# Kernel tuning notes

Hardware: AMD Instinct MI355X
Metric: run time of the kernel (lower is better)

The kernel has to match this reference:

```python
import jax, jax.numpy as jnp
import numpy as np

B, N, H, S, C = 32, 64, 128, 100, 16
SIGMA = 0.5  # perturbations.perturbed default noise scale


def setup_inputs() -> dict:
    key = jax.random.key(0)
    ks = jax.random.split(key, 8)
    x = jax.random.normal(ks[0], (B, N, H), jnp.float32)
    a = (jax.random.uniform(ks[1], (B, N, N)) < 0.1).astype(jnp.float32)
    adj = jnp.maximum(a, jnp.swapaxes(a, -1, -2))  # symmetric binary adjacency
    counts = jax.random.randint(ks[2], (B,), N // 2, N + 1)
    mask = jnp.arange(N)[None, :] < counts[:, None]
    sc = 1.0 / np.sqrt(H).astype(np.float32)
    W1 = jax.random.normal(ks[3], (H, H), jnp.float32) * sc
    b1 = jnp.zeros((H,), jnp.float32)
    W2 = jax.random.normal(ks[4], (H, H), jnp.float32) * sc
    b2 = jnp.zeros((H,), jnp.float32)
    cW1 = jax.random.normal(ks[5], (H, H), jnp.float32) * sc
    cb1 = jnp.zeros((H,), jnp.float32)
    cW2 = jax.random.normal(ks[6], (H, C), jnp.float32) * sc
    cb2 = jnp.zeros((C,), jnp.float32)
    noise = jax.random.normal(ks[7], (S * B, N, H), jnp.float32)
    return dict(x=x, adj=adj, mask=mask, W1=W1, b1=b1, W2=W2, b2=b2,
                cW1=cW1, cb1=cb1, cW2=cW2, cb2=cb2, noise=noise, num_samples=S)


def _gcn(x, adj, mask, W, b):
    # DenseGCNConv: set diag to 1, symmetric-normalize, propagate, mask.
    h = x @ W
    n = adj.shape[-1]
    eye = jnp.eye(n, dtype=bool)
    a = jnp.where(eye, 1.0, adj)
    d = jnp.clip(a.sum(-1), 1.0, None) ** -0.5
    a = d[..., :, None] * a * d[..., None, :]
    out = a @ h + b
    return out * mask[..., None].astype(out.dtype)


def _perturbed_clustering(x_all, adj_all, mask_all, cW1, cb1, cW2, cb2):
    BS, n, h = x_all.shape
    # concept MLP + argmax
    logits = jax.nn.relu(x_all @ cW1 + cb1) @ cW2 + cb2
    concepts = jnp.argmax(logits, axis=-1)  # [BS, n]
    same = concepts[:, :, None] == concepts[:, None, :]
    adj_c = jnp.where(same, adj_all, 0.0)
    # connected components via min-label propagation (scipy-order relabel)
    edge = (adj_c > 0) & mask_all[:, :, None] & mask_all[:, None, :]
    labels0 = jnp.where(mask_all, jnp.arange(n, dtype=jnp.int32), n)

    def body(_, labels):
        neigh = jnp.min(jnp.where(edge, labels[:, None, :], n), axis=-1)
        return jnp.minimum(labels, neigh)

    roots = jax.lax.fori_loop(0, n, body, labels0)  # min node idx of component
    present = jnp.zeros((BS, n + 1), jnp.int32).at[
        jnp.arange(BS)[:, None], roots].max(mask_all.astype(jnp.int32))
    rank = jnp.cumsum(present[:, :n], axis=-1)  # 1-based compact id per root
    assignments = jnp.where(
        mask_all,
        jnp.take_along_axis(rank, jnp.minimum(roots, n - 1), axis=-1), 0)
    # scatter-reduce pooling; segment ids flatten (batch, cluster); slot 0 = masked
    seg = (jnp.arange(BS, dtype=jnp.int32)[:, None] * (n + 1) + assignments).reshape(-1)
    x_new = jax.ops.segment_sum(x_all.reshape(BS * n, h), seg,
                                num_segments=BS * (n + 1)).reshape(BS, n + 1, h)[:, 1:]
    row = jax.ops.segment_max(adj_all.reshape(BS * n, n), seg,
                              num_segments=BS * (n + 1)).reshape(BS, n + 1, n)[:, 1:]
    row = jnp.maximum(row, 0.0)  # torch_scatter max includes zero-init
    colsrc = jnp.swapaxes(row, 1, 2).reshape(BS * n, n)
    adj_new = jax.ops.segment_max(colsrc, seg,
                                  num_segments=BS * (n + 1)).reshape(BS, n + 1, n)[:, 1:]
    adj_new = jnp.maximum(jnp.swapaxes(adj_new, 1, 2), 0.0)
    num_clusters = jnp.max(assignments, axis=-1)
    mask_new = jnp.arange(n)[None, :] < num_clusters[:, None]
    return x_new, adj_new, mask_new, assignments


def reference(x, adj, mask, W1, b1, W2, b2, cW1, cb1, cW2, cb2, noise, num_samples):
    # embedding GCN stack
    xe = jax.nn.relu(_gcn(x, adj, mask, W1, b1))
    x_emb = jax.nn.relu(_gcn(xe, adj, mask, W2, b2))
    Bb, n, h = x_emb.shape
    # perturbed replication (sample-major layout, matching final reshape(S, -1, ...))
    adj_all = jnp.tile(adj, (num_samples, 1, 1))
    mask_all = jnp.tile(mask, (num_samples, 1))
    x_all = jnp.tile(x_emb, (num_samples, 1, 1)) + SIGMA * noise
    x_new, adj_new, mask_new, assignments = _perturbed_clustering(
        x_all, adj_all, mask_all, cW1, cb1, cW2, cb2)
    # perturbed expectation for x_new; explicit mean/max in forward for adj/mask
    x_new = x_new.reshape(num_samples, Bb, n, h).mean(axis=0)
    adj_new = adj_new.reshape(num_samples, Bb, n, n).mean(axis=0)
    mask_new = jnp.max(mask_new.reshape(num_samples, Bb, n), axis=0)
    return x_new, adj_new, assignments, x_emb, mask_new
```

## Files before the change

### kernel.cpp

```cpp
#include <hip/hip_runtime.h>
#include <cstdint>

#define B_ 32
#define N_ 64
#define H_ 128
#define S_ 100
#define C_ 16
#define SIGMA_ 0.5f

#define OFF_XNEW 0
#define OFF_ADJN 262144
#define OFF_ASGN 393216
#define OFF_XEMB 598016
#define OFF_MSKN 860160

__device__ __forceinline__ int read_mask_elem(const void* mp, int idx) {
    const unsigned int* u = (const unsigned int*)mp;
    const unsigned int w0 = u[0], w1 = u[1];
    if (w0 == 1u) {
        if (w1 == 1u) return ((const int*)mp)[idx] != 0;
        return ((const int*)mp)[2 * idx] != 0;
    }
    if (w0 == 0x3f800000u) return ((const float*)mp)[idx] != 0.0f;
    if (w0 == 0u) return ((const double*)mp)[idx] != 0.0;
    return ((const unsigned char*)mp)[idx] != 0;
}

__global__ __launch_bounds__(256) void gcn_kernel(
    const float* __restrict__ x, const float* __restrict__ adj,
    const void* __restrict__ maskp,
    const float* __restrict__ W1, const float* __restrict__ b1,
    const float* __restrict__ W2, const float* __restrict__ b2,
    float* __restrict__ out,
    unsigned long long* __restrict__ abits_ws,
    unsigned long long* __restrict__ mbits_ws)
{
    const int b = blockIdx.x;
    const int t = threadIdx.x;
    __shared__ float Xs[N_][130];
    __shared__ float Hs[N_][130];
    __shared__ float An[N_][65];
    __shared__ float dsh[N_];
    __shared__ unsigned long long mb_sh;

    if (t < 64) {
        const int mv = read_mask_elem(maskp, b * N_ + t);
        const unsigned long long bal = __ballot(mv != 0);
        if (t == 0) { mb_sh = bal; mbits_ws[b] = bal; }
    }
    for (int row = (t >> 6); row < N_; row += 4) {
        const int j = t & 63;
        const float v = adj[((size_t)b * N_ + row) * N_ + j];
        const unsigned long long bal = __ballot(v > 0.0f);
        if (j == 0) abits_ws[b * N_ + row] = bal;
        An[row][j] = (row == j) ? 1.0f : v;
    }
    __syncthreads();
    if (t < 64) {
        float s = 0.0f;
        for (int j = 0; j < N_; ++j) s += An[t][j];
        if (s < 1.0f) s = 1.0f;
        dsh[t] = 1.0f / sqrtf(s);
    }
    __syncthreads();
    for (int e = t; e < N_ * N_; e += 256) {
        const int i = e >> 6, j = e & 63;
        An[i][j] *= dsh[i] * dsh[j];
    }
    for (int e = t; e < N_ * H_; e += 256)
        Xs[e >> 7][e & 127] = x[(size_t)b * N_ * H_ + e];
    __syncthreads();

    const int ng = t & 15, kg = t >> 4;
    const unsigned long long mb = mb_sh;

    {
        float acc[4][8] = {};
        for (int d = 0; d < H_; ++d) {
            float xv[4];
#pragma unroll
            for (int r = 0; r < 4; ++r) xv[r] = Xs[4 * ng + r][d];
            const float4 wa = *(const float4*)(W1 + d * H_ + 8 * kg);
            const float4 wb = *(const float4*)(W1 + d * H_ + 8 * kg + 4);
            const float wf[8] = {wa.x, wa.y, wa.z, wa.w, wb.x, wb.y, wb.z, wb.w};
#pragma unroll
            for (int j = 0; j < 8; ++j)
#pragma unroll
                for (int r = 0; r < 4; ++r) acc[r][j] += xv[r] * wf[j];
        }
#pragma unroll
        for (int r = 0; r < 4; ++r)
#pragma unroll
            for (int j = 0; j < 8; ++j) Hs[4 * ng + r][8 * kg + j] = acc[r][j];
    }
    __syncthreads();
    {
        float acc[4][8] = {};
        for (int j2 = 0; j2 < N_; ++j2) {
            float av[4];
#pragma unroll
            for (int r = 0; r < 4; ++r) av[r] = An[4 * ng + r][j2];
            float hv[8];
#pragma unroll
            for (int j = 0; j < 8; ++j) hv[j] = Hs[j2][8 * kg + j];
#pragma unroll
            for (int j = 0; j < 8; ++j)
#pragma unroll
                for (int r = 0; r < 4; ++r) acc[r][j] += av[r] * hv[j];
        }
        const float4 ba = *(const float4*)(b1 + 8 * kg);
        const float4 bb = *(const float4*)(b1 + 8 * kg + 4);
        const float bf[8] = {ba.x, ba.y, ba.z, ba.w, bb.x, bb.y, bb.z, bb.w};
#pragma unroll
        for (int r = 0; r < 4; ++r) {
            const int i = 4 * ng + r;
            const float m = ((mb >> i) & 1ull) ? 1.0f : 0.0f;
#pragma unroll
            for (int j = 0; j < 8; ++j)
                Xs[i][8 * kg + j] = fmaxf(acc[r][j] + bf[j], 0.0f) * m;
        }
    }
    __syncthreads();
    {
        float acc[4][8] = {};
        for (int d = 0; d < H_; ++d) {
            float xv[4];
#pragma unroll
            for (int r = 0; r < 4; ++r) xv[r] = Xs[4 * ng + r][d];
            const float4 wa = *(const float4*)(W2 + d * H_ + 8 * kg);
            const float4 wb = *(const float4*)(W2 + d * H_ + 8 * kg + 4);
            const float wf[8] = {wa.x, wa.y, wa.z, wa.w, wb.x, wb.y, wb.z, wb.w};
#pragma unroll
            for (int j = 0; j < 8; ++j)
#pragma unroll
                for (int r = 0; r < 4; ++r) acc[r][j] += xv[r] * wf[j];
        }
        __syncthreads();
#pragma unroll
        for (int r = 0; r < 4; ++r)
#pragma unroll
            for (int j = 0; j < 8; ++j) Hs[4 * ng + r][8 * kg + j] = acc[r][j];
    }
    __syncthreads();
    {
        float acc[4][8] = {};
        for (int j2 = 0; j2 < N_; ++j2) {
            float av[4];
#pragma unroll
            for (int r = 0; r < 4; ++r) av[r] = An[4 * ng + r][j2];
            float hv[8];
#pragma unroll
            for (int j = 0; j < 8; ++j) hv[j] = Hs[j2][8 * kg + j];
#pragma unroll
            for (int j = 0; j < 8; ++j)
#pragma unroll
                for (int r = 0; r < 4; ++r) acc[r][j] += av[r] * hv[j];
        }
        const float4 ba = *(const float4*)(b2 + 8 * kg);
        const float4 bb = *(const float4*)(b2 + 8 * kg + 4);
        const float bf[8] = {ba.x, ba.y, ba.z, ba.w, bb.x, bb.y, bb.z, bb.w};
#pragma unroll
        for (int r = 0; r < 4; ++r) {
            const int i = 4 * ng + r;
            const float m = ((mb >> i) & 1ull) ? 1.0f : 0.0f;
#pragma unroll
            for (int j = 0; j < 8; ++j)
                out[OFF_XEMB + (size_t)b * N_ * H_ + i * H_ + 8 * kg + j] =
                    fmaxf(acc[r][j] + bf[j], 0.0f) * m;
        }
    }
}

__device__ __forceinline__ float rscat16(float* v, int kg) {
#pragma unroll
    for (int i = 0; i < 8; ++i) {
        const float send = (kg & 8) ? v[i] : v[i + 8];
        const float recv = __shfl_xor(send, 8);
        v[i] = ((kg & 8) ? v[i + 8] : v[i]) + recv;
    }
#pragma unroll
    for (int i = 0; i < 4; ++i) {
        const float send = (kg & 4) ? v[i] : v[i + 4];
        const float recv = __shfl_xor(send, 4);
        v[i] = ((kg & 4) ? v[i + 4] : v[i]) + recv;
    }
#pragma unroll
    for (int i = 0; i < 2; ++i) {
        const float send = (kg & 2) ? v[i] : v[i + 2];
        const float recv = __shfl_xor(send, 2);
        v[i] = ((kg & 2) ? v[i + 2] : v[i]) + recv;
    }
    {
        const float send = (kg & 1) ? v[0] : v[1];
        const float recv = __shfl_xor(send, 1);
        v[0] = ((kg & 1) ? v[1] : v[0]) + recv;
    }
    return v[0];
}

__device__ __forceinline__ void argmax16(float bv, int kg, int* dst) {
    int bi = kg;
#pragma unroll
    for (int m = 1; m <= 8; m <<= 1) {
        const float ov = __shfl_xor(bv, m);
        const int   oi = __shfl_xor(bi, m);
        if (ov > bv || (ov == bv && oi < bi)) { bv = ov; bi = oi; }
    }
    if (kg == 0) *dst = bi;
}

__global__ __launch_bounds__(256) void sample_kernel(
    const float* __restrict__ noise,
    const float* __restrict__ cW1, const float* __restrict__ cb1,
    const float* __restrict__ cW2, const float* __restrict__ cb2,
    const unsigned long long* __restrict__ abits_ws,
    const unsigned long long* __restrict__ mbits_ws,
    float* __restrict__ out, int* __restrict__ gNcl)
{
    const int sb = blockIdx.x;
    const int b  = sb & (B_ - 1);
    const int t  = threadIdx.x;
    __shared__ float xa[N_ * H_];
    __shared__ int   concepts[N_];
    __shared__ unsigned long long reachL[N_];
    __shared__ unsigned long long cmS[N_];
    __shared__ unsigned long long roS[N_];
    __shared__ unsigned long long abS[N_];
    __shared__ unsigned int presLo, presHi;

    const unsigned long long mb = mbits_ws[b];
    if (t < 64) abS[t] = abits_ws[b * N_ + t];
    if (t == 0) { presLo = 0u; presHi = 0u; }

    {
        const float4* e4 = (const float4*)(out + OFF_XEMB + (size_t)b * N_ * H_);
        const float4* n4 = (const float4*)(noise + (size_t)sb * N_ * H_);
        float4* x4 = (float4*)xa;
        for (int idx = t; idx < N_ * 32; idx += 256) {
            const int i = idx >> 5, cc = idx & 31;
            const float4 ev = e4[idx], nv = n4[idx];
            float4 v;
            v.x = ev.x + SIGMA_ * nv.x;  v.y = ev.y + SIGMA_ * nv.y;
            v.z = ev.z + SIGMA_ * nv.z;  v.w = ev.w + SIGMA_ * nv.w;
            x4[i * 32 + (cc ^ (i & 7))] = v;
        }
    }
    __syncthreads();

    const int ng = t >> 4, kg = t & 15;
    float acc[4][8] = {};
    {
        const float4* x4 = (const float4*)xa;
        const int swzb = 4 * (ng & 1);
        for (int cc = 0; cc < 32; ++cc) {
            float xv[4][4];
#pragma unroll
            for (int r = 0; r < 4; ++r) {
                const float4 tmp = x4[(4 * ng + r) * 32 + (cc ^ (swzb + r))];
                xv[r][0] = tmp.x; xv[r][1] = tmp.y; xv[r][2] = tmp.z; xv[r][3] = tmp.w;
            }
#pragma unroll
            for (int dd = 0; dd < 4; ++dd) {
                const int d = cc * 4 + dd;
                const float4 wa = *(const float4*)(cW1 + d * H_ + 8 * kg);
                const float4 wb = *(const float4*)(cW1 + d * H_ + 8 * kg + 4);
                const float wf[8] = {wa.x, wa.y, wa.z, wa.w, wb.x, wb.y, wb.z, wb.w};
#pragma unroll
                for (int j = 0; j < 8; ++j)
#pragma unroll
                    for (int r = 0; r < 4; ++r) acc[r][j] += xv[r][dd] * wf[j];
            }
        }
    }
    {
        const float4 ba = *(const float4*)(cb1 + 8 * kg);
        const float4 bb = *(const float4*)(cb1 + 8 * kg + 4);
        const float bf[8] = {ba.x, ba.y, ba.z, ba.w, bb.x, bb.y, bb.z, bb.w};
        const float cb2v = cb2[kg];
#pragma unroll
        for (int r = 0; r < 4; ++r) {
            float h[8];
#pragma unroll
            for (int j = 0; j < 8; ++j) h[j] = fmaxf(acc[r][j] + bf[j], 0.0f);
            float pl[16] = {};
#pragma unroll
            for (int j = 0; j < 8; ++j) {
                const float4* w2r = (const float4*)(cW2 + (8 * kg + j) * C_);
                const float4 w0 = w2r[0], w1 = w2r[1], w2v = w2r[2], w3 = w2r[3];
                const float wf2[16] = {w0.x, w0.y, w0.z, w0.w, w1.x, w1.y, w1.z, w1.w,
                                       w2v.x, w2v.y, w2v.z, w2v.w, w3.x, w3.y, w3.z, w3.w};
#pragma unroll
                for (int c = 0; c < C_; ++c) pl[c] += h[j] * wf2[c];
            }
            const float l = rscat16(pl, kg) + cb2v;
            argmax16(l, kg, &concepts[4 * ng + r]);
        }
    }
    __syncthreads();

    unsigned long long reach = 0ull;
    int masked_i = 0;
    if (t < 64) {
        masked_i = (int)((mb >> t) & 1ull);
        if (masked_i) {
            const int ci = concepts[t];
            unsigned long long mm = abS[t] & mb;
            unsigned long long em = 0ull;
            while (mm) {
                const int j = __builtin_ctzll(mm);
                if (concepts[j] == ci) em |= (1ull << j);
                mm &= mm - 1;
            }
            reach = em | (1ull << t);
        }
        reachL[t] = reach;
    }
    __syncthreads();
    for (;;) {
        unsigned long long r = reach;
        if (masked_i) {
            unsigned long long mm = reach & ~(1ull << t);
            while (mm) {
                const int j = __builtin_ctzll(mm);
                r |= reachL[j];
                mm &= mm - 1;
            }
        }
        const int changed = (r != reach);
        __syncthreads();
        if (t < 64) reachL[t] = r;
        reach = r;
        if (!__syncthreads_or(changed)) break;
    }
    int root = 0;
    if (masked_i) {
        root = __builtin_ctzll(reach);
        if (root < 32) atomicOr(&presLo, 1u << root);
        else           atomicOr(&presHi, 1u << (root - 32));
    }
    __syncthreads();
    const unsigned long long present =
        ((unsigned long long)presHi << 32) | (unsigned long long)presLo;
    const int ncl = __popcll(present);
    if (t < 64) {
        int a_i = 0;
        if (masked_i) {
            a_i = __popcll(present & ((1ull << root) - 1ull)) + 1;
            if (root == t) {
                cmS[a_i - 1] = reach;
                unsigned long long ro = 0ull, mm = reach;
                while (mm) { const int j = __builtin_ctzll(mm); ro |= abS[j]; mm &= mm - 1; }
                roS[a_i - 1] = ro;
            }
        }
        out[OFF_ASGN + (size_t)sb * N_ + t] = (float)a_i;
    }
    __syncthreads();

    for (int e = t; e < ncl * H_; e += 256) {
        const int c = e >> 7, d = e & 127;
        unsigned long long mm = cmS[c];
        float s = 0.0f;
        while (mm) {
            const int j = __builtin_ctzll(mm);
            s += xa[j * H_ + ((((d >> 2) ^ (j & 7)) << 2) | (d & 3))];
            mm &= mm - 1;
        }
        atomicAdd(&out[OFF_XNEW + (size_t)b * N_ * H_ + e], s);
    }
    {
        int* adjCnt = (int*)out + OFF_ADJN;
        for (int idx = t; idx < ncl * N_; idx += 256) {
            const int c1 = idx >> 6, c2 = idx & 63;
            if (c2 < ncl && (roS[c1] & cmS[c2]))
                atomicAdd(&adjCnt[b * N_ * N_ + idx], 1);
        }
    }
    if (t == 0) atomicMax(&gNcl[b], ncl);
}

__global__ __launch_bounds__(256) void finalize_kernel(
    float* __restrict__ out, const int* __restrict__ gNcl)
{
    const int idx = blockIdx.x * 256 + threadIdx.x;
    if (idx < OFF_ADJN) {
        out[idx] = out[idx] / 100.0f;
    } else if (idx < OFF_ASGN) {
        const int c = ((const int*)out)[idx];
        out[idx] = (float)c / 100.0f;
    } else {
        const int m = idx - OFF_ASGN;
        if (m < B_ * N_) {
            const int bb = m >> 6, k = m & 63;
            out[OFF_MSKN + m] = (k < gNcl[bb]) ? 1.0f : 0.0f;
        }
    }
}

extern "C" void kernel_launch(void* const* d_in, const int* in_sizes, int n_in,
                              void* d_out, int out_size, void* d_ws, size_t ws_size,
                              hipStream_t stream) {
    (void)in_sizes; (void)n_in; (void)out_size; (void)ws_size;
    const float* x    = (const float*)d_in[0];
    const float* adj  = (const float*)d_in[1];
    const void*  mskp = d_in[2];
    const float* W1   = (const float*)d_in[3];
    const float* b1   = (const float*)d_in[4];
    const float* W2   = (const float*)d_in[5];
    const float* b2   = (const float*)d_in[6];
    const float* cW1  = (const float*)d_in[7];
    const float* cb1  = (const float*)d_in[8];
    const float* cW2  = (const float*)d_in[9];
    const float* cb2  = (const float*)d_in[10];
    const float* noise = (const float*)d_in[11];
    float* out = (float*)d_out;

    int* gNcl = (int*)d_ws;
    unsigned long long* abits_ws = (unsigned long long*)((char*)d_ws + 256);
    unsigned long long* mbits_ws = (unsigned long long*)((char*)d_ws + 256 + 16384);

    hipMemsetAsync(d_out, 0, (size_t)OFF_ASGN * sizeof(float), stream);
    hipMemsetAsync(d_ws, 0, 256, stream);

    gcn_kernel<<<B_, 256, 0, stream>>>(x, adj, mskp, W1, b1, W2, b2,
                                       out, abits_ws, mbits_ws);
    sample_kernel<<<S_ * B_, 256, 0, stream>>>(noise, cW1, cb1, cW2, cb2,
                                               abits_ws, mbits_ws, out, gNcl);
    finalize_kernel<<<(OFF_ASGN + B_ * N_ + 255) / 256, 256, 0, stream>>>(out, gNcl);
}
```

Before: 528.3 us.

## Split pipeline into staged kernels with atomic-free bf16 partial reduction

The single GCN kernel becomes two gcn_stage launches, each spread across 8 column chunks per graph, so more blocks run in parallel. The monolithic sample kernel is split into separate MLP/argmax, clustering (one wavefront per sample), pooling and reduction kernels. Global float and int atomics for x_new and adjacency counts are replaced by per-sample bf16 partial sums and bit-packed adjacency rows, which a final kernel reduces. This removes atomic contention and the memsets, at the cost of more launches, re-reading the noise in the pool stage, tens of MB of workspace traffic, and bf16 rounding of the partial sums.

```diff
diff --git a/kernel.cpp b/kernel.cpp
--- a/kernel.cpp
+++ b/kernel.cpp
@@ -14,6 +14,25 @@
 #define OFF_XEMB 598016
 #define OFF_MSKN 860160
 
+#define WS_NCL_OFF   0
+#define WS_ABITS_OFF 16384
+#define WS_MBITS_OFF 32768
+#define WS_CONC_OFF  65536
+#define WS_CM_OFF    917504
+#define WS_ADJB_OFF  2555904
+#define WS_XE_OFF    4194304
+#define WS_PART_OFF  5242880
+#define WS_NEED      57671680ull
+
+__device__ __forceinline__ unsigned short f2bf(float f) {
+    unsigned int u = __float_as_uint(f);
+    u += 0x7fffu + ((u >> 16) & 1u);
+    return (unsigned short)(u >> 16);
+}
+__device__ __forceinline__ float bf2f(unsigned short h) {
+    return __uint_as_float(((unsigned int)h) << 16);
+}
+
 __device__ __forceinline__ int read_mask_elem(const void* mp, int idx) {
     const unsigned int* u = (const unsigned int*)mp;
     const unsigned int w0 = u[0], w1 = u[1];
@@ -26,35 +45,37 @@
     return ((const unsigned char*)mp)[idx] != 0;
 }
 
-__global__ __launch_bounds__(256) void gcn_kernel(
-    const float* __restrict__ x, const float* __restrict__ adj,
+__global__ __launch_bounds__(256) void gcn_stage(
+    const float* __restrict__ Xin, const float* __restrict__ adj,
     const void* __restrict__ maskp,
-    const float* __restrict__ W1, const float* __restrict__ b1,
-    const float* __restrict__ W2, const float* __restrict__ b2,
-    float* __restrict__ out,
+    const float* __restrict__ W, const float* __restrict__ bias,
+    float* __restrict__ Xout,
     unsigned long long* __restrict__ abits_ws,
-    unsigned long long* __restrict__ mbits_ws)
+    unsigned long long* __restrict__ mbits_ws, int emit_bits)
 {
-    const int b = blockIdx.x;
+    const int b = blockIdx.x, cc = blockIdx.y;
     const int t = threadIdx.x;
-    __shared__ float Xs[N_][130];
-    __shared__ float Hs[N_][130];
+    const int tj = t & 63, tc = t >> 6;
+    __shared__ float Xs[N_][129];
     __shared__ float An[N_][65];
+    __shared__ float Hc[N_][20];
     __shared__ float dsh[N_];
     __shared__ unsigned long long mb_sh;
 
     if (t < 64) {
         const int mv = read_mask_elem(maskp, b * N_ + t);
         const unsigned long long bal = __ballot(mv != 0);
-        if (t == 0) { mb_sh = bal; mbits_ws[b] = bal; }
+        if (t == 0) { mb_sh = bal; if (emit_bits && cc == 0) mbits_ws[b] = bal; }
     }
     for (int row = (t >> 6); row < N_; row += 4) {
         const int j = t & 63;
         const float v = adj[((size_t)b * N_ + row) * N_ + j];
         const unsigned long long bal = __ballot(v > 0.0f);
-        if (j == 0) abits_ws[b * N_ + row] = bal;
+        if (emit_bits && cc == 0 && j == 0) abits_ws[b * N_ + row] = bal;
         An[row][j] = (row == j) ? 1.0f : v;
     }
+    for (int e = t; e < N_ * H_; e += 256)
+        Xs[e >> 7][e & 127] = Xin[(size_t)b * N_ * H_ + e];
     __syncthreads();
     if (t < 64) {
         float s = 0.0f;
@@ -67,107 +88,31 @@
         const int i = e >> 6, j = e & 63;
         An[i][j] *= dsh[i] * dsh[j];
     }
-    for (int e = t; e < N_ * H_; e += 256)
-        Xs[e >> 7][e & 127] = x[(size_t)b * N_ * H_ + e];
-    __syncthreads();
-
-    const int ng = t & 15, kg = t >> 4;
-    const unsigned long long mb = mb_sh;
-
-    {
-        float acc[4][8] = {};
+    {
+        float a0 = 0, a1 = 0, a2 = 0, a3 = 0;
+        const float* wp = W + cc * 16 + tc * 4;
         for (int d = 0; d < H_; ++d) {
-            float xv[4];
-#pragma unroll
-            for (int r = 0; r < 4; ++r) xv[r] = Xs[4 * ng + r][d];
-            const float4 wa = *(const float4*)(W1 + d * H_ + 8 * kg);
-            const float4 wb = *(const float4*)(W1 + d * H_ + 8 * kg + 4);
-            const float wf[8] = {wa.x, wa.y, wa.z, wa.w, wb.x, wb.y, wb.z, wb.w};
-#pragma unroll
-            for (int j = 0; j < 8; ++j)
-#pragma unroll
-                for (int r = 0; r < 4; ++r) acc[r][j] += xv[r] * wf[j];
-        }
-#pragma unroll
-        for (int r = 0; r < 4; ++r)
-#pragma unroll
-            for (int j = 0; j < 8; ++j) Hs[4 * ng + r][8 * kg + j] = acc[r][j];
-    }
-    __syncthreads();
-    {
-        float acc[4][8] = {};
+            const float xv = Xs[tj][d];
+            const float4 w = *(const float4*)(wp + d * H_);
+            a0 += xv * w.x; a1 += xv * w.y; a2 += xv * w.z; a3 += xv * w.w;
+        }
+        float4 o; o.x = a0; o.y = a1; o.z = a2; o.w = a3;
+        *(float4*)&Hc[tj][tc * 4] = o;
+    }
+    __syncthreads();
+    {
+        float c0 = 0, c1 = 0, c2 = 0, c3 = 0;
         for (int j2 = 0; j2 < N_; ++j2) {
-            float av[4];
-#pragma unroll
-            for (int r = 0; r < 4; ++r) av[r] = An[4 * ng + r][j2];
-            float hv[8];
-#pragma unroll
-            for (int j = 0; j < 8; ++j) hv[j] = Hs[j2][8 * kg + j];
-#pragma unroll
-            for (int j = 0; j < 8; ++j)
-#pragma unroll
-                for (int r = 0; r < 4; ++r) acc[r][j] += av[r] * hv[j];
-        }
-        const float4 ba = *(const float4*)(b1 + 8 * kg);
-        const float4 bb = *(const float4*)(b1 + 8 * kg + 4);
-        const float bf[8] = {ba.x, ba.y, ba.z, ba.w, bb.x, bb.y, bb.z, bb.w};
-#pragma unroll
-        for (int r = 0; r < 4; ++r) {
-            const int i = 4 * ng + r;
-            const float m = ((mb >> i) & 1ull) ? 1.0f : 0.0f;
-#pragma unroll
-            for (int j = 0; j < 8; ++j)
-                Xs[i][8 * kg + j] = fmaxf(acc[r][j] + bf[j], 0.0f) * m;
-        }
-    }
-    __syncthreads();
-    {
-        float acc[4][8] = {};
-        for (int d = 0; d < H_; ++d) {
-            float xv[4];
-#pragma unroll
-            for (int r = 0; r < 4; ++r) xv[r] = Xs[4 * ng + r][d];
-            const float4 wa = *(const float4*)(W2 + d * H_ + 8 * kg);
-            const float4 wb = *(const float4*)(W2 + d * H_ + 8 * kg + 4);
-            const float wf[8] = {wa.x, wa.y, wa.z, wa.w, wb.x, wb.y, wb.z, wb.w};
-#pragma unroll
-            for (int j = 0; j < 8; ++j)
-#pragma unroll
-                for (int r = 0; r < 4; ++r) acc[r][j] += xv[r] * wf[j];
-        }
-        __syncthreads();
-#pragma unroll
-        for (int r = 0; r < 4; ++r)
-#pragma unroll
-            for (int j = 0; j < 8; ++j) Hs[4 * ng + r][8 * kg + j] = acc[r][j];
-    }
-    __syncthreads();
-    {
-        float acc[4][8] = {};
-        for (int j2 = 0; j2 < N_; ++j2) {
-            float av[4];
-#pragma unroll
-            for (int r = 0; r < 4; ++r) av[r] = An[4 * ng + r][j2];
-            float hv[8];
-#pragma unroll
-            for (int j = 0; j < 8; ++j) hv[j] = Hs[j2][8 * kg + j];
-#pragma unroll
-            for (int j = 0; j < 8; ++j)
-#pragma unroll
-                for (int r = 0; r < 4; ++r) acc[r][j] += av[r] * hv[j];
-        }
-        const float4 ba = *(const float4*)(b2 + 8 * kg);
-        const float4 bb = *(const float4*)(b2 + 8 * kg + 4);
-        const float bf[8] = {ba.x, ba.y, ba.z, ba.w, bb.x, bb.y, bb.z, bb.w};
-#pragma unroll
-        for (int r = 0; r < 4; ++r) {
-            const int i = 4 * ng + r;
-            const float m = ((mb >> i) & 1ull) ? 1.0f : 0.0f;
-#pragma unroll
-            for (int j = 0; j < 8; ++j)
-                out[OFF_XEMB + (size_t)b * N_ * H_ + i * H_ + 8 * kg + j] =
-                    fmaxf(acc[r][j] + bf[j], 0.0f) * m;
-        }
+            const float av = An[tj][j2];
+            const float4 h = *(const float4*)&Hc[j2][tc * 4];
+            c0 += av * h.x; c1 += av * h.y; c2 += av * h.z; c3 += av * h.w;
+        }
+        const float4 bq = *(const float4*)(bias + cc * 16 + tc * 4);
+        const float m = ((mb_sh >> tj) & 1ull) ? 1.0f : 0.0f;
+        float4 o;
+        o.x = fmaxf(c0 + bq.x, 0.0f) * m; o.y = fmaxf(c1 + bq.y, 0.0f) * m;
+        o.z = fmaxf(c2 + bq.z, 0.0f) * m; o.w = fmaxf(c3 + bq.w, 0.0f) * m;
+        *(float4*)&Xout[(size_t)b * N_ * H_ + tj * H_ + cc * 16 + tc * 4] = o;
     }
 }
 
@@ -209,31 +154,19 @@
     if (kg == 0) *dst = bi;
 }
 
-__global__ __launch_bounds__(256) void sample_kernel(
-    const float* __restrict__ noise,
+__global__ __launch_bounds__(256) void mlp_kernel(
+    const float* __restrict__ xemb, const float* __restrict__ noise,
     const float* __restrict__ cW1, const float* __restrict__ cb1,
     const float* __restrict__ cW2, const float* __restrict__ cb2,
-    const unsigned long long* __restrict__ abits_ws,
-    const unsigned long long* __restrict__ mbits_ws,
-    float* __restrict__ out, int* __restrict__ gNcl)
+    int* __restrict__ conc)
 {
     const int sb = blockIdx.x;
     const int b  = sb & (B_ - 1);
     const int t  = threadIdx.x;
     __shared__ float xa[N_ * H_];
-    __shared__ int   concepts[N_];
-    __shared__ unsigned long long reachL[N_];
-    __shared__ unsigned long long cmS[N_];
-    __shared__ unsigned long long roS[N_];
-    __shared__ unsigned long long abS[N_];
-    __shared__ unsigned int presLo, presHi;
-
-    const unsigned long long mb = mbits_ws[b];
-    if (t < 64) abS[t] = abits_ws[b * N_ + t];
-    if (t == 0) { presLo = 0u; presHi = 0u; }
-
-    {
-        const float4* e4 = (const float4*)(out + OFF_XEMB + (size_t)b * N_ * H_);
+
+    {
+        const float4* e4 = (const float4*)(xemb + (size_t)b * N_ * H_);
         const float4* n4 = (const float4*)(noise + (size_t)sb * N_ * H_);
         float4* x4 = (float4*)xa;
         for (int idx = t; idx < N_ * 32; idx += 256) {
@@ -293,107 +226,150 @@
                 for (int c = 0; c < C_; ++c) pl[c] += h[j] * wf2[c];
             }
             const float l = rscat16(pl, kg) + cb2v;
-            argmax16(l, kg, &concepts[4 * ng + r]);
-        }
-    }
-    __syncthreads();
-
+            argmax16(l, kg, conc + sb * N_ + 4 * ng + r);
+        }
+    }
+}
+
+__global__ __launch_bounds__(256) void cluster_kernel(
+    const int* __restrict__ conc,
+    const unsigned long long* __restrict__ abits_ws,
+    const unsigned long long* __restrict__ mbits_ws,
+    unsigned long long* __restrict__ cm_ws,
+    unsigned long long* __restrict__ adjbits,
+    int* __restrict__ nclArr, float* __restrict__ asgn_out)
+{
+    const int w = threadIdx.x >> 6, lane = threadIdx.x & 63;
+    const int sb = blockIdx.x * 4 + w;
+    const int b = sb & (B_ - 1);
+    __shared__ int cl[4][N_];
+    __shared__ unsigned long long reachL[4][N_];
+    __shared__ unsigned long long cmL[4][N_];
+    __shared__ unsigned long long roL[4][N_];
+    __shared__ unsigned long long abL[4][N_];
+
+    const unsigned long long mb = mbits_ws[b];
+    const unsigned long long abv = abits_ws[b * N_ + lane];
+    cl[w][lane] = conc[sb * N_ + lane];
+    abL[w][lane] = abv;
+    cmL[w][lane] = 0ull; roL[w][lane] = 0ull;
+    __syncthreads();
+
+    const int masked = (int)((mb >> lane) & 1ull);
     unsigned long long reach = 0ull;
-    int masked_i = 0;
-    if (t < 64) {
-        masked_i = (int)((mb >> t) & 1ull);
-        if (masked_i) {
-            const int ci = concepts[t];
-            unsigned long long mm = abS[t] & mb;
-            unsigned long long em = 0ull;
+    if (masked) {
+        const int ci = cl[w][lane];
+        unsigned long long mm = abv & mb, em = 0ull;
+        while (mm) {
+            const int j = __builtin_ctzll(mm);
+            if (cl[w][j] == ci) em |= (1ull << j);
+            mm &= mm - 1;
+        }
+        reach = em | (1ull << lane);
+    }
+    reachL[w][lane] = reach;
+    __syncthreads();
+    for (;;) {
+        unsigned long long r = reach;
+        if (masked) {
+            unsigned long long mm = reach & ~(1ull << lane);
             while (mm) {
                 const int j = __builtin_ctzll(mm);
-                if (concepts[j] == ci) em |= (1ull << j);
+                r |= reachL[w][j];
                 mm &= mm - 1;
             }
-            reach = em | (1ull << t);
-        }
-        reachL[t] = reach;
-    }
-    __syncthreads();
-    for (;;) {
-        unsigned long long r = reach;
-        if (masked_i) {
-            unsigned long long mm = reach & ~(1ull << t);
-            while (mm) {
-                const int j = __builtin_ctzll(mm);
-                r |= reachL[j];
-                mm &= mm - 1;
-            }
         }
         const int changed = (r != reach);
         __syncthreads();
-        if (t < 64) reachL[t] = r;
+        reachL[w][lane] = r;
         reach = r;
         if (!__syncthreads_or(changed)) break;
     }
-    int root = 0;
-    if (masked_i) {
-        root = __builtin_ctzll(reach);
-        if (root < 32) atomicOr(&presLo, 1u << root);
-        else           atomicOr(&presHi, 1u << (root - 32));
-    }
-    __syncthreads();
-    const unsigned long long present =
-        ((unsigned long long)presHi << 32) | (unsigned long long)presLo;
+    const int root = masked ? __builtin_ctzll(reach) : 0;
+    const unsigned long long present = __ballot(masked && (root == lane));
     const int ncl = __popcll(present);
-    if (t < 64) {
-        int a_i = 0;
-        if (masked_i) {
-            a_i = __popcll(present & ((1ull << root) - 1ull)) + 1;
-            if (root == t) {
-                cmS[a_i - 1] = reach;
-                unsigned long long ro = 0ull, mm = reach;
-                while (mm) { const int j = __builtin_ctzll(mm); ro |= abS[j]; mm &= mm - 1; }
-                roS[a_i - 1] = ro;
-            }
-        }
-        out[OFF_ASGN + (size_t)sb * N_ + t] = (float)a_i;
-    }
-    __syncthreads();
-
-    for (int e = t; e < ncl * H_; e += 256) {
-        const int c = e >> 7, d = e & 127;
-        unsigned long long mm = cmS[c];
-        float s = 0.0f;
+    const int a_i = masked ? (__popcll(present & ((1ull << root) - 1ull)) + 1) : 0;
+    if (masked && root == lane) {
+        unsigned long long ro = 0ull, mm = reach;
+        while (mm) { const int j = __builtin_ctzll(mm); ro |= abL[w][j]; mm &= mm - 1; }
+        cmL[w][a_i - 1] = reach;
+        roL[w][a_i - 1] = ro;
+    }
+    __syncthreads();
+    asgn_out[(size_t)sb * N_ + lane] = (float)a_i;
+    cm_ws[(size_t)sb * N_ + lane] = cmL[w][lane];
+    unsigned long long row = 0ull;
+    if (lane < ncl) {
+        const unsigned long long ro = roL[w][lane];
+        for (int c2 = 0; c2 < ncl; ++c2)
+            if (ro & cmL[w][c2]) row |= (1ull << c2);
+    }
+    adjbits[(size_t)sb * N_ + lane] = row;
+    if (lane == 0) nclArr[sb] = ncl;
+}
+
+__global__ __launch_bounds__(256) void pool_kernel(
+    const float* __restrict__ xemb, const float* __restrict__ noise,
+    const unsigned long long* __restrict__ cm_ws,
+    unsigned short* __restrict__ part)
+{
+    const int sb = blockIdx.x;
+    const int b  = sb & (B_ - 1);
+    const int t  = threadIdx.x;
+    const float4* e4 = (const float4*)(xemb + (size_t)b * N_ * H_);
+    const float4* n4 = (const float4*)(noise + (size_t)sb * N_ * H_);
+    for (int e = t; e < N_ * 32; e += 256) {
+        const int c = e >> 5, d4 = e & 31;
+        unsigned long long mm = cm_ws[(size_t)sb * N_ + c];
+        float4 s = {0.f, 0.f, 0.f, 0.f};
         while (mm) {
             const int j = __builtin_ctzll(mm);
-            s += xa[j * H_ + ((((d >> 2) ^ (j & 7)) << 2) | (d & 3))];
+            const float4 ev = e4[j * 32 + d4];
+            const float4 nv = n4[j * 32 + d4];
+            s.x += ev.x + SIGMA_ * nv.x; s.y += ev.y + SIGMA_ * nv.y;
+            s.z += ev.z + SIGMA_ * nv.z; s.w += ev.w + SIGMA_ * nv.w;
             mm &= mm - 1;
         }
-        atomicAdd(&out[OFF_XNEW + (size_t)b * N_ * H_ + e], s);
-    }
-    {
-        int* adjCnt = (int*)out + OFF_ADJN;
-        for (int idx = t; idx < ncl * N_; idx += 256) {
-            const int c1 = idx >> 6, c2 = idx & 63;
-            if (c2 < ncl && (roS[c1] & cmS[c2]))
-                atomicAdd(&adjCnt[b * N_ * N_ + idx], 1);
-        }
-    }
-    if (t == 0) atomicMax(&gNcl[b], ncl);
-}
-
-__global__ __launch_bounds__(256) void finalize_kernel(
-    float* __restrict__ out, const int* __restrict__ gNcl)
+        ushort4 o;
+        o.x = f2bf(s.x); o.y = f2bf(s.y); o.z = f2bf(s.z); o.w = f2bf(s.w);
+        *(ushort4*)&part[(size_t)sb * (N_ * H_) + e * 4] = o;
+    }
+}
+
+__global__ __launch_bounds__(256) void reduce_kernel(
+    const unsigned short* __restrict__ part,
+    const unsigned long long* __restrict__ adjbits,
+    const int* __restrict__ nclArr, float* __restrict__ out)
 {
     const int idx = blockIdx.x * 256 + threadIdx.x;
-    if (idx < OFF_ADJN) {
-        out[idx] = out[idx] / 100.0f;
-    } else if (idx < OFF_ASGN) {
-        const int c = ((const int*)out)[idx];
-        out[idx] = (float)c / 100.0f;
-    } else {
-        const int m = idx - OFF_ASGN;
-        if (m < B_ * N_) {
-            const int bb = m >> 6, k = m & 63;
-            out[OFF_MSKN + m] = (k < gNcl[bb]) ? 1.0f : 0.0f;
-        }
+    if (idx < 65536) {
+        const int b = idx >> 11, rem = idx & 2047;
+        float4 s = {0.f, 0.f, 0.f, 0.f};
+        const unsigned short* p = part + (size_t)b * (N_ * H_) + rem * 4;
+#pragma unroll 4
+        for (int s_ = 0; s_ < S_; ++s_) {
+            const ushort4 v = *(const ushort4*)(p + (size_t)s_ * (B_ * N_ * H_));
+            s.x += bf2f(v.x); s.y += bf2f(v.y); s.z += bf2f(v.z); s.w += bf2f(v.w);
+        }
+        s.x *= 0.01f; s.y *= 0.01f; s.z *= 0.01f; s.w *= 0.01f;
+        *(float4*)&out[OFF_XNEW + (size_t)b * (N_ * H_) + rem * 4] = s;
+    } else if (idx < 65536 + 131072) {
+        const int j = idx - 65536;
+        const int b = j >> 12, c1 = (j >> 6) & 63, c2 = j & 63;
+        int cnt = 0;
+#pragma unroll 4
+        for (int s_ = 0; s_ < S_; ++s_)
+            cnt += (int)((adjbits[((size_t)s_ * B_ + b) * N_ + c1] >> c2) & 1ull);
+        out[OFF_ADJN + j] = (float)cnt * 0.01f;
+    } else if (idx < 65536 + 131072 + 2048) {
+        const int m = idx - 196608;
+        const int b = m >> 6, k = m & 63;
+        int mx = 0;
+        for (int s_ = 0; s_ < S_; ++s_) {
+            const int v = nclArr[s_ * B_ + b];
+            mx = v > mx ? v : mx;
+        }
+        out[OFF_MSKN + m] = (k < mx) ? 1.0f : 0.0f;
     }
 }
 
@@ -415,16 +391,26 @@
     const float* noise = (const float*)d_in[11];
     float* out = (float*)d_out;
 
-    int* gNcl = (int*)d_ws;
-    unsigned long long* abits_ws = (unsigned long long*)((char*)d_ws + 256);
-    unsigned long long* mbits_ws = (unsigned long long*)((char*)d_ws + 256 + 16384);
-
-    hipMemsetAsync(d_out, 0, (size_t)OFF_ASGN * sizeof(float), stream);
-    hipMemsetAsync(d_ws, 0, 256, stream);
-
-    gcn_kernel<<<B_, 256, 0, stream>>>(x, adj, mskp, W1, b1, W2, b2,
-                                       out, abits_ws, mbits_ws);
-    sample_kernel<<<S_ * B_, 256, 0, stream>>>(noise, cW1, cb1, cW2, cb2,
-                                               abits_ws, mbits_ws, out, gNcl);
-    finalize_kernel<<<(OFF_ASGN + B_ * N_ + 255) / 256, 256, 0, stream>>>(out, gNcl);
-}
+    int* nclArr = (int*)d_ws;
+    unsigned long long* abits_ws = (unsigned long long*)((char*)d_ws + WS_ABITS_OFF);
+    unsigned long long* mbits_ws = (unsigned long long*)((char*)d_ws + WS_MBITS_OFF);
+    int* conc = (int*)((char*)d_ws + WS_CONC_OFF);
+    unsigned long long* cm_ws = (unsigned long long*)((char*)d_ws + WS_CM_OFF);
+    unsigned long long* adjbits = (unsigned long long*)((char*)d_ws + WS_ADJB_OFF);
+    float* xe_ws = (float*)((char*)d_ws + WS_XE_OFF);
+    unsigned short* part = (unsigned short*)((char*)d_ws + WS_PART_OFF);
+
+    float* xemb = out + OFF_XEMB;
+
+    gcn_stage<<<dim3(B_, 8), 256, 0, stream>>>(x, adj, mskp, W1, b1, xe_ws,
+                                               abits_ws, mbits_ws, 1);
+    gcn_stage<<<dim3(B_, 8), 256, 0, stream>>>(xe_ws, adj, mskp, W2, b2, xemb,
+                                               abits_ws, mbits_ws, 0);
+    mlp_kernel<<<S_ * B_, 256, 0, stream>>>(xemb, noise, cW1, cb1, cW2, cb2, conc);
+    cluster_kernel<<<S_ * B_ / 4, 256, 0, stream>>>(conc, abits_ws, mbits_ws,
+                                                    cm_ws, adjbits, nclArr,
+                                                    out + OFF_ASGN);
+    pool_kernel<<<S_ * B_, 256, 0, stream>>>(xemb, noise, cm_ws, part);
+    reduce_kernel<<<(65536 + 131072 + 2048) / 256, 256, 0, stream>>>(
+        part, adjbits, nclArr, out);
+}
```

After: 519.1 us. Within noise of the previous version (-1.8%).
